# Kernel tuning notes

Measured on AMD Instinct MI355X. Metric: run time of the kernel, lower is better.

Reference implementation:

```python
import math
import jax, jax.numpy as jnp
import numpy as np

B, S, D, H, L = 2, 2048, 1024, 16, 4
HD = D // H  # head_dim = 64


def setup_inputs() -> dict:
    key = jax.random.key(0)
    ks = jax.random.split(key, 7)
    scale = 0.02
    return {
        "x": jax.random.normal(ks[0], (B, S, D), jnp.float32),
        "past_q": jax.random.normal(ks[1], (B, H, S, L, HD), jnp.float32),
        "past_v": jax.random.normal(ks[2], (B, H, S, L, HD), jnp.float32),
        "Wq": jax.random.normal(ks[3], (D, D), jnp.float32) * scale,
        "bq": jnp.zeros((D,), jnp.float32),
        "Wo": jax.random.normal(ks[4], (D, D), jnp.float32) * scale,
        "bo": jnp.zeros((D,), jnp.float32),
    }


def reference(x, past_q, past_v, Wq, bq, Wo, bo):
    b, s, d = x.shape
    # q_proj then split heads -> [B,H,S,hd]
    q = (x @ Wq.T + bq).reshape(b, s, H, HD).transpose(0, 2, 1, 3)
    v = x.reshape(b, s, H, HD).transpose(0, 2, 1, 3)
    inv = 1.0 / math.sqrt(HD)
    # token scores: Q used as both query and key, causal mask
    token_scores = jnp.einsum("bhqd,bhkd->bhqk", q, q) * inv
    causal = jnp.triu(jnp.ones((s, s), bool), k=1)
    token_scores = jnp.where(causal, -jnp.inf, token_scores)
    # memory scores: elementwise mul-sum over L cached layers -> [B,H,S,L]
    mem_scores = jnp.einsum("bhsd,bhsld->bhsl", q, past_q) * inv
    scores = jnp.concatenate([token_scores, mem_scores], axis=-1)  # [B,H,S,S+L]
    weights = jax.nn.softmax(scores, axis=-1)
    tw, mw = weights[..., :s], weights[..., s:]
    token_ctx = jnp.einsum("bhqk,bhkd->bhqd", tw, v)
    mem_ctx = jnp.einsum("bhsl,bhsld->bhsd", mw, past_v)
    ctx = (token_ctx + mem_ctx).transpose(0, 2, 1, 3).reshape(b, s, d)
    return jax.nn.gelu(ctx @ Wo.T + bo, approximate=False)
```

## Files before the change

kernel.cpp:

```cpp
#include <hip/hip_runtime.h>
#include <hip/hip_bf16.h>
#include <math.h>

#define S_LEN 2048
#define DIM   1024
#define NH    16
#define NL    4
#define NB    2
#define PARTS_PER_BH 80
#define ALPHA 0.42466086f

typedef __attribute__((ext_vector_type(8))) short bf16x8;
typedef __attribute__((ext_vector_type(4))) float f32x4;
typedef unsigned short u16;

__device__ __forceinline__ float bf2f(u16 u) {
  union { unsigned int i; float f; } x; x.i = ((unsigned int)u) << 16; return x.f;
}
__device__ __forceinline__ u16 f2bf(float f) {
  union { float f; unsigned int i; } x; x.f = f;
  unsigned int r = x.i + 0x7fffu + ((x.i >> 16) & 1u);
  return (u16)(r >> 16);
}
__device__ __forceinline__ u16 f2bfq(float f) {
  __hip_bfloat16 h = __float2bfloat16(f);
  return *reinterpret_cast<u16*>(&h);
}

__device__ __forceinline__ void g2l16(const void* g, void* l) {
  __builtin_amdgcn_global_load_lds(
      (const __attribute__((address_space(1))) void*)g,
      (__attribute__((address_space(3))) void*)l, 16, 0, 0);
}

__global__ __launch_bounds__(256)
void cvt_all(const float* __restrict__ x, const float* __restrict__ wq,
             const float* __restrict__ wo, u16* __restrict__ ox,
             u16* __restrict__ owq, u16* __restrict__ owo, int n4x, int n4w) {
  int i = blockIdx.x * blockDim.x + threadIdx.x;
  const float* src; u16* dst; int j;
  if (i < n4x)            { src = x;  dst = ox;  j = i; }
  else if (i < n4x + n4w) { src = wq; dst = owq; j = i - n4x; }
  else                    { src = wo; dst = owo; j = i - n4x - n4w;
                            if (j >= n4w) return; }
  float4 v = ((const float4*)src)[j];
  ushort4 o;
  o.x = f2bf(v.x); o.y = f2bf(v.y); o.z = f2bf(v.z); o.w = f2bf(v.w);
  ((ushort4*)dst)[j] = o;
}

template <bool GELU, typename OT>
__global__ __launch_bounds__(256)
void gemm_bt(const u16* __restrict__ A, const u16* __restrict__ Bt,
             const float* __restrict__ bias, OT* __restrict__ C,
             int M, int N, int K, float oscale) {
  __shared__ u16 As[128 * 64];
  __shared__ u16 Bs[64 * 64];
  const int lane = threadIdx.x & 63, wave = threadIdx.x >> 6;
  const int ln = lane & 15, g = lane >> 4;
  const int m0 = blockIdx.y * 128, n0 = blockIdx.x * 64;
  const int wm = wave >> 1, wn = wave & 1;
  f32x4 acc[4][2] = {};

  for (int k0 = 0; k0 < K; k0 += 64) {
    __syncthreads();
#pragma unroll
    for (int rd = 0; rd < 6; ++rd) {
      int ch = rd * 4 + wave;
      if (ch < 16) {
        int flat = ch * 1024 + lane * 16;
        int row = flat >> 7;
        int within = (flat & 127) ^ ((row & 7) << 4);
        g2l16((const char*)A + ((size_t)(m0 + row) * K + k0) * 2 + within,
              (char*)As + ch * 1024);
      } else {
        int flat = (ch - 16) * 1024 + lane * 16;
        int row = flat >> 7;
        int within = (flat & 127) ^ ((row & 7) << 4);
        g2l16((const char*)Bt + ((size_t)(n0 + row) * K + k0) * 2 + within,
              (char*)Bs + (ch - 16) * 1024);
      }
    }
    __syncthreads();
#pragma unroll
    for (int kc = 0; kc < 2; ++kc) {
      bf16x8 af[4], bfr[2];
#pragma unroll
      for (int i = 0; i < 4; ++i) {
        int ra = wm * 64 + i * 16 + ln;
        af[i] = *(const bf16x8*)((const char*)As + ra * 128 +
                                 ((kc * 64 + g * 16) ^ ((ra & 7) << 4)));
      }
#pragma unroll
      for (int j = 0; j < 2; ++j) {
        int rb = wn * 32 + j * 16 + ln;
        bfr[j] = *(const bf16x8*)((const char*)Bs + rb * 128 +
                                  ((kc * 64 + g * 16) ^ ((rb & 7) << 4)));
      }
#pragma unroll
      for (int i = 0; i < 4; ++i)
#pragma unroll
        for (int j = 0; j < 2; ++j)
          acc[i][j] = __builtin_amdgcn_mfma_f32_16x16x32_bf16(af[i], bfr[j], acc[i][j], 0, 0, 0);
    }
  }

#pragma unroll
  for (int j = 0; j < 2; ++j) {
    int gc = n0 + wn * 32 + j * 16 + ln;
    float bv = bias[gc];
#pragma unroll
    for (int i = 0; i < 4; ++i) {
      int gr0 = m0 + wm * 64 + i * 16 + g * 4;
#pragma unroll
      for (int r = 0; r < 4; ++r) {
        float v = acc[i][j][r] + bv;
        if constexpr (GELU) v = 0.5f * v * (1.0f + erff(v * 0.70710678118f));
        v *= oscale;
        if constexpr (sizeof(OT) == 2) C[(size_t)(gr0 + r) * N + gc] = (OT)f2bf(v);
        else                           C[(size_t)(gr0 + r) * N + gc] = (OT)v;
      }
    }
  }
}

__global__ __launch_bounds__(256)
void attn(const u16* __restrict__ Q, const u16* __restrict__ Xb,
          u16* __restrict__ CTXP, float* __restrict__ MP, float* __restrict__ LP) {
  __shared__ u16 Ks[2][64 * 64];
  __shared__ u16 Vt[2][64 * 64];
  __shared__ u16 Pw[4][16 * 64];

  const int lane = threadIdx.x & 63, wave = threadIdx.x >> 6;
  const int ln = lane & 15, g = lane >> 4;
  const int h = blockIdx.y, b = blockIdx.z;

  const int p = blockIdx.x;
  int qt, chunk;
  if (p < 8)       { qt = p;                          chunk = 0; }
  else if (p < 24) { int i = p - 8;  qt = 8 + (i >> 1);  chunk = i & 1; }
  else if (p < 48) { int i = p - 24; qt = 16 + i / 3;    chunk = i % 3; }
  else             { int i = p - 48; qt = 24 + (i >> 2); chunk = i & 3; }
  const int kt0 = chunk * 8;
  const int kt1e = kt0 + 8 < qt + 1 ? kt0 + 8 : qt + 1;

  const size_t qrow = (size_t)b * S_LEN + qt * 64 + wave * 16 + ln;
  const bf16x8 qa0 = *(const bf16x8*)(Q + qrow * DIM + h * 64 + g * 8);
  const bf16x8 qa1 = *(const bf16x8*)(Q + qrow * DIM + h * 64 + 32 + g * 8);

  f32x4 acc[4] = {};
  float m_run = -INFINITY;
  float l_run = 0.f;

  const int tid = threadIdx.x;
  const int vr0 = (tid >> 3) * 2;
  const int vc0 = (tid & 7) * 8;
#define VSWZ(c) ((((c) ^ ((c) >> 3)) & 7) << 4)

  {
    const u16* xsrc = Xb + ((size_t)b * S_LEN + kt0 * 64 + vr0) * DIM + h * 64 + vc0;
    bf16x8 r0 = *(const bf16x8*)xsrc;
    bf16x8 r1 = *(const bf16x8*)(xsrc + DIM);
#pragma unroll
    for (int rd = 0; rd < 2; ++rd) {
      int ch = rd * 4 + wave;
      int flat = ch * 1024 + lane * 16;
      int row = flat >> 7;
      int within = (flat & 127) ^ ((row & 7) << 4);
      g2l16((const char*)Q + (((size_t)b * S_LEN + kt0 * 64 + row) * DIM + h * 64) * 2 + within,
            (char*)Ks[0] + ch * 1024);
    }
#pragma unroll
    for (int j = 0; j < 8; ++j) {
      int c = vc0 + j;
      unsigned int pack = (unsigned int)(u16)r0[j] | ((unsigned int)(u16)r1[j] << 16);
      *(unsigned int*)((char*)Vt[0] + c * 128 + ((vr0 * 2) ^ VSWZ(c))) = pack;
    }
  }
  __syncthreads();

  for (int kt = kt0; kt < kt1e; ++kt) {
    const int cur = (kt - kt0) & 1, nxt = cur ^ 1;
    const bool more = (kt + 1 < kt1e);
    bf16x8 nr0, nr1;
    if (more) {
      const u16* xsrc = Xb + ((size_t)b * S_LEN + (kt + 1) * 64 + vr0) * DIM + h * 64 + vc0;
      nr0 = *(const bf16x8*)xsrc;
      nr1 = *(const bf16x8*)(xsrc + DIM);
#pragma unroll
      for (int rd = 0; rd < 2; ++rd) {
        int ch = rd * 4 + wave;
        int flat = ch * 1024 + lane * 16;
        int row = flat >> 7;
        int within = (flat & 127) ^ ((row & 7) << 4);
        g2l16((const char*)Q + (((size_t)b * S_LEN + (kt + 1) * 64 + row) * DIM + h * 64) * 2 + within,
              (char*)Ks[nxt] + ch * 1024);
      }
      __builtin_amdgcn_sched_barrier(0);
    }

    float pv_[4][4];
#pragma unroll
    for (int sub = 0; sub < 4; ++sub) {
      int kr = sub * 16 + ln;
      bf16x8 kb0 = *(const bf16x8*)((const char*)Ks[cur] + kr * 128 + ((g * 16) ^ ((kr & 7) << 4)));
      bf16x8 kb1 = *(const bf16x8*)((const char*)Ks[cur] + kr * 128 + ((64 + g * 16) ^ ((kr & 7) << 4)));
      f32x4 c = {};
      c = __builtin_amdgcn_mfma_f32_16x16x32_bf16(kb0, qa0, c, 0, 0, 0);
      c = __builtin_amdgcn_mfma_f32_16x16x32_bf16(kb1, qa1, c, 0, 0, 0);
      if (kt == qt) {
#pragma unroll
        for (int r = 0; r < 4; ++r) {
          int key = sub * 16 + g * 4 + r;
          int qi = wave * 16 + ln;
          pv_[sub][r] = (key > qi) ? -INFINITY : c[r];
        }
      } else {
#pragma unroll
        for (int r = 0; r < 4; ++r) pv_[sub][r] = c[r];
      }
    }

    float pmax = pv_[0][0];
#pragma unroll
    for (int sub = 0; sub < 4; ++sub)
#pragma unroll
      for (int r = 0; r < 4; ++r) pmax = fmaxf(pmax, pv_[sub][r]);
    pmax = fmaxf(pmax, __shfl_xor(pmax, 16));
    pmax = fmaxf(pmax, __shfl_xor(pmax, 32));

    if (!__all(pmax <= m_run + 8.0f)) {
      float m_new = fmaxf(m_run, pmax);
      float scl = exp2f(m_run - m_new);
      m_run = m_new;
      l_run *= scl;
#pragma unroll
      for (int r = 0; r < 4; ++r) {
        float s = __shfl(scl, g * 4 + r);
#pragma unroll
        for (int ns = 0; ns < 4; ++ns) acc[ns][r] *= s;
      }
    }

    float lsum = 0.f;
#pragma unroll
    for (int sub = 0; sub < 4; ++sub)
#pragma unroll
      for (int r = 0; r < 4; ++r) {
        pv_[sub][r] = exp2f(pv_[sub][r] - m_run);
        lsum += pv_[sub][r];
      }
    lsum += __shfl_xor(lsum, 16);
    lsum += __shfl_xor(lsum, 32);
    l_run += lsum;

#pragma unroll
    for (int sub = 0; sub < 4; ++sub) {
      uint2 val;
      val.x = (unsigned int)f2bfq(pv_[sub][0]) | ((unsigned int)f2bfq(pv_[sub][1]) << 16);
      val.y = (unsigned int)f2bfq(pv_[sub][2]) | ((unsigned int)f2bfq(pv_[sub][3]) << 16);
      *(uint2*)((char*)Pw[wave] + ln * 128 + ((sub * 32 + g * 8) ^ ((ln & 7) << 4))) = val;
    }

    bf16x8 pa0 = *(const bf16x8*)((const char*)Pw[wave] + ln * 128 + ((g * 16) ^ ((ln & 7) << 4)));
    bf16x8 pa1 = *(const bf16x8*)((const char*)Pw[wave] + ln * 128 + ((64 + g * 16) ^ ((ln & 7) << 4)));
#pragma unroll
    for (int ns = 0; ns < 4; ++ns) {
      int vr = ns * 16 + ln;
      bf16x8 vb0 = *(const bf16x8*)((const char*)Vt[cur] + vr * 128 + ((g * 16) ^ VSWZ(vr)));
      bf16x8 vb1 = *(const bf16x8*)((const char*)Vt[cur] + vr * 128 + ((64 + g * 16) ^ VSWZ(vr)));
      acc[ns] = __builtin_amdgcn_mfma_f32_16x16x32_bf16(pa0, vb0, acc[ns], 0, 0, 0);
      acc[ns] = __builtin_amdgcn_mfma_f32_16x16x32_bf16(pa1, vb1, acc[ns], 0, 0, 0);
    }

    if (more) {
#pragma unroll
      for (int j = 0; j < 8; ++j) {
        int c = vc0 + j;
        unsigned int pack = (unsigned int)(u16)nr0[j] | ((unsigned int)(u16)nr1[j] << 16);
        *(unsigned int*)((char*)Vt[nxt] + c * 128 + ((vr0 * 2) ^ VSWZ(c))) = pack;
      }
    }
    __syncthreads();
  }

  const size_t slot = ((size_t)(b * NH + h)) * PARTS_PER_BH + p;
#pragma unroll
  for (int ns = 0; ns < 4; ++ns)
#pragma unroll
    for (int r = 0; r < 4; ++r) {
      int qr = wave * 16 + g * 4 + r;
      CTXP[slot * 4096 + (size_t)qr * 64 + ns * 16 + ln] = f2bfq(acc[ns][r]);
    }
  if (lane < 16) {
    MP[slot * 64 + wave * 16 + lane] = m_run;
    LP[slot * 64 + wave * 16 + lane] = l_run;
  }
}

__global__ __launch_bounds__(256)
void finalize(const u16* __restrict__ Q, const float* __restrict__ PQ,
              const float* __restrict__ PV, const u16* __restrict__ CTXP,
              const float* __restrict__ MP, const float* __restrict__ LP,
              u16* __restrict__ Cout) {
  const int lane = threadIdx.x & 63, wave = threadIdx.x >> 6;
  const size_t row = (size_t)blockIdx.x * 4 + wave;
  const int s = (int)(row & (S_LEN - 1));
  const int h = (int)((row >> 11) & (NH - 1));
  const int b = (int)(row >> 15);

  const int qt = s >> 6, G = qt >> 3, parts = G + 1;
  const int baseG[4] = {0, 8, 24, 48};
  const int p0 = baseG[G] + (qt & 7) * parts;
  const size_t slot0 = ((size_t)(b * NH + h)) * PARTS_PER_BH + p0;
  const int sr = s & 63;

  float mc[4], lc[4];
  float m_tok = -INFINITY;
#pragma unroll
  for (int c = 0; c < 4; ++c)
    if (c < parts) {
      mc[c] = MP[(slot0 + c) * 64 + sr];
      lc[c] = LP[(slot0 + c) * 64 + sr];
      m_tok = fmaxf(m_tok, mc[c]);
    }
  float l_tok = 0.f, cd = 0.f;
#pragma unroll
  for (int c = 0; c < 4; ++c)
    if (c < parts) {
      float w = exp2f(mc[c] - m_tok);
      l_tok += w * lc[c];
      cd += w * bf2f(CTXP[(slot0 + c) * 4096 + (size_t)sr * 64 + lane]);
    }

  const float qd = bf2f(Q[((size_t)b * S_LEN + s) * DIM + h * 64 + lane]);
  const float* pq = PQ + row * (NL * 64);
  const float* pv = PV + row * (NL * 64);
  float msc[NL];
  float m_fin = m_tok;
#pragma unroll
  for (int lm = 0; lm < NL; ++lm) {
    float prod = qd * pq[lm * 64 + lane];
#pragma unroll
    for (int o = 1; o < 64; o <<= 1) prod += __shfl_xor(prod, o);
    msc[lm] = prod * ALPHA;
    m_fin = fmaxf(m_fin, msc[lm]);
  }
  const float a = exp2f(m_tok - m_fin);
  float l_fin = l_tok * a;
  cd *= a;
#pragma unroll
  for (int lm = 0; lm < NL; ++lm) {
    float w = exp2f(msc[lm] - m_fin);
    l_fin += w;
    cd += w * pv[lm * 64 + lane];
  }
  Cout[((size_t)b * S_LEN + s) * DIM + h * 64 + lane] = f2bf(cd / l_fin);
}

extern "C" void kernel_launch(void* const* d_in, const int* in_sizes, int n_in,
                              void* d_out, int out_size, void* d_ws, size_t ws_size,
                              hipStream_t stream) {
  const float* x  = (const float*)d_in[0];
  const float* pq = (const float*)d_in[1];
  const float* pv = (const float*)d_in[2];
  const float* Wq = (const float*)d_in[3];
  const float* bq = (const float*)d_in[4];
  const float* Wo = (const float*)d_in[5];
  const float* bo = (const float*)d_in[6];
  float* out = (float*)d_out;

  const int M = NB * S_LEN;
  u16*   Qws  = (u16*)d_ws;
  u16*   Cws  = Qws + (size_t)M * DIM;
  u16*   xbf  = Cws + (size_t)M * DIM;
  u16*   Wqbf = xbf + (size_t)M * DIM;
  u16*   Wobf = Wqbf + (size_t)DIM * DIM;
  u16*   CTXP = Wobf + (size_t)DIM * DIM;
  float* MP   = (float*)(CTXP + (size_t)NB * NH * PARTS_PER_BH * 4096);
  float* LP   = MP + (size_t)NB * NH * PARTS_PER_BH * 64;

  const int n4x = M * DIM / 4, n4w = DIM * DIM / 4;
  cvt_all<<<(n4x + 2 * n4w + 255) / 256, 256, 0, stream>>>(
      x, Wq, Wo, xbf, Wqbf, Wobf, n4x, n4w);

  gemm_bt<false, u16><<<dim3(DIM / 64, M / 128), 256, 0, stream>>>(
      xbf, Wqbf, bq, Qws, M, DIM, DIM, ALPHA);
  attn<<<dim3(PARTS_PER_BH, NH, NB), 256, 0, stream>>>(Qws, xbf, CTXP, MP, LP);
  finalize<<<NB * NH * S_LEN / 4, 256, 0, stream>>>(Qws, pq, pv, CTXP, MP, LP, Cws);
  gemm_bt<true, float><<<dim3(DIM / 64, M / 128), 256, 0, stream>>>(
      Cws, Wobf, bo, out, M, DIM, DIM, 1.0f);
}
```

Measured before the change: 137.8 us.

## Double-buffer GEMM LDS tiles and defer softmax cross-lane reductions in attention

The GEMM kernel now keeps two LDS buffers, loading the next K tile while MFMAs consume the current one, which removes one barrier per iteration and overlaps global loads with compute. In the attention kernel the per-row max is only combined across lanes when a rescale is triggered, and the row-sum is kept per lane and reduced once after the loop. This removes shuffles from the hot loop. Double buffering doubles GEMM LDS use, which may lower occupancy.

```diff
diff --git a/kernel.cpp b/kernel.cpp
--- a/kernel.cpp
+++ b/kernel.cpp
@@ -54,16 +54,15 @@
 void gemm_bt(const u16* __restrict__ A, const u16* __restrict__ Bt,
              const float* __restrict__ bias, OT* __restrict__ C,
              int M, int N, int K, float oscale) {
-  __shared__ u16 As[128 * 64];
-  __shared__ u16 Bs[64 * 64];
+  __shared__ u16 As[2][128 * 64];
+  __shared__ u16 Bs[2][64 * 64];
   const int lane = threadIdx.x & 63, wave = threadIdx.x >> 6;
   const int ln = lane & 15, g = lane >> 4;
   const int m0 = blockIdx.y * 128, n0 = blockIdx.x * 64;
   const int wm = wave >> 1, wn = wave & 1;
   f32x4 acc[4][2] = {};
 
-  for (int k0 = 0; k0 < K; k0 += 64) {
-    __syncthreads();
+  auto stage = [&](int buf, int k0) {
 #pragma unroll
     for (int rd = 0; rd < 6; ++rd) {
       int ch = rd * 4 + wave;
@@ -72,29 +71,36 @@
         int row = flat >> 7;
         int within = (flat & 127) ^ ((row & 7) << 4);
         g2l16((const char*)A + ((size_t)(m0 + row) * K + k0) * 2 + within,
-              (char*)As + ch * 1024);
+              (char*)As[buf] + ch * 1024);
       } else {
         int flat = (ch - 16) * 1024 + lane * 16;
         int row = flat >> 7;
         int within = (flat & 127) ^ ((row & 7) << 4);
         g2l16((const char*)Bt + ((size_t)(n0 + row) * K + k0) * 2 + within,
-              (char*)Bs + (ch - 16) * 1024);
-      }
-    }
-    __syncthreads();
+              (char*)Bs[buf] + (ch - 16) * 1024);
+      }
+    }
+  };
+
+  stage(0, 0);
+  __syncthreads();
+  const int NT = K / 64;
+  for (int t = 0; t < NT; ++t) {
+    const int cur = t & 1;
+    if (t + 1 < NT) stage(cur ^ 1, (t + 1) * 64);
 #pragma unroll
     for (int kc = 0; kc < 2; ++kc) {
       bf16x8 af[4], bfr[2];
 #pragma unroll
       for (int i = 0; i < 4; ++i) {
         int ra = wm * 64 + i * 16 + ln;
-        af[i] = *(const bf16x8*)((const char*)As + ra * 128 +
+        af[i] = *(const bf16x8*)((const char*)As[cur] + ra * 128 +
                                  ((kc * 64 + g * 16) ^ ((ra & 7) << 4)));
       }
 #pragma unroll
       for (int j = 0; j < 2; ++j) {
         int rb = wn * 32 + j * 16 + ln;
-        bfr[j] = *(const bf16x8*)((const char*)Bs + rb * 128 +
+        bfr[j] = *(const bf16x8*)((const char*)Bs[cur] + rb * 128 +
                                   ((kc * 64 + g * 16) ^ ((rb & 7) << 4)));
       }
 #pragma unroll
@@ -103,6 +109,7 @@
         for (int j = 0; j < 2; ++j)
           acc[i][j] = __builtin_amdgcn_mfma_f32_16x16x32_bf16(af[i], bfr[j], acc[i][j], 0, 0, 0);
     }
+    __syncthreads();
   }
 
 #pragma unroll
@@ -150,7 +157,7 @@
 
   f32x4 acc[4] = {};
   float m_run = -INFINITY;
-  float l_run = 0.f;
+  float l_part = 0.f;
 
   const int tid = threadIdx.x;
   const int vr0 = (tid >> 3) * 2;
@@ -221,19 +228,21 @@
       }
     }
 
-    float pmax = pv_[0][0];
-#pragma unroll
-    for (int sub = 0; sub < 4; ++sub)
-#pragma unroll
-      for (int r = 0; r < 4; ++r) pmax = fmaxf(pmax, pv_[sub][r]);
-    pmax = fmaxf(pmax, __shfl_xor(pmax, 16));
-    pmax = fmaxf(pmax, __shfl_xor(pmax, 32));
+    float t0 = fmaxf(fmaxf(pv_[0][0], pv_[0][1]), pv_[0][2]);
+    float t1 = fmaxf(fmaxf(pv_[0][3], pv_[1][0]), pv_[1][1]);
+    float t2 = fmaxf(fmaxf(pv_[1][2], pv_[1][3]), pv_[2][0]);
+    float t3 = fmaxf(fmaxf(pv_[2][1], pv_[2][2]), pv_[2][3]);
+    float t4 = fmaxf(fmaxf(pv_[3][0], pv_[3][1]), pv_[3][2]);
+    float pmax = fmaxf(fmaxf(fmaxf(t0, t1), fmaxf(t2, t3)),
+                       fmaxf(t4, pv_[3][3]));
 
     if (!__all(pmax <= m_run + 8.0f)) {
-      float m_new = fmaxf(m_run, pmax);
+      float fm = fmaxf(pmax, __shfl_xor(pmax, 16));
+      fm = fmaxf(fm, __shfl_xor(fm, 32));
+      float m_new = fmaxf(m_run, fm);
       float scl = exp2f(m_run - m_new);
       m_run = m_new;
-      l_run *= scl;
+      l_part *= scl;
 #pragma unroll
       for (int r = 0; r < 4; ++r) {
         float s = __shfl(scl, g * 4 + r);
@@ -242,17 +251,15 @@
       }
     }
 
-    float lsum = 0.f;
+    float ls = 0.f;
 #pragma unroll
     for (int sub = 0; sub < 4; ++sub)
 #pragma unroll
       for (int r = 0; r < 4; ++r) {
         pv_[sub][r] = exp2f(pv_[sub][r] - m_run);
-        lsum += pv_[sub][r];
-      }
-    lsum += __shfl_xor(lsum, 16);
-    lsum += __shfl_xor(lsum, 32);
-    l_run += lsum;
+        ls += pv_[sub][r];
+      }
+    l_part += ls;
 
 #pragma unroll
     for (int sub = 0; sub < 4; ++sub) {
@@ -283,6 +290,10 @@
     }
     __syncthreads();
   }
+
+  float l_run = l_part;
+  l_run += __shfl_xor(l_run, 16);
+  l_run += __shfl_xor(l_run, 32);
 
   const size_t slot = ((size_t)(b * NH + h)) * PARTS_PER_BH + p;
 #pragma unroll
```

New measurement: 142.7 us. +3.6%, slower.

## Double-buffer GEMM LDS tiles and load attention K directly from global memory

Applied to the files above, without the earlier changes.

The GEMM now double-buffers its A/B shared-memory tiles, issuing the next K-tile's async loads before computing on the current one, so there is one barrier per iteration instead of two. In the attention kernel the K tile is no longer staged through LDS; each lane reads its K fragments straight from global memory (Q), which removes the LDS traffic and shared-memory footprint. The trade-off is that global-load latency now sits directly in front of the QK^T MFMAs with no prefetch, and the GEMM uses twice the LDS, which may reduce occupancy.

```diff
diff --git a/kernel.cpp b/kernel.cpp
--- a/kernel.cpp
+++ b/kernel.cpp
@@ -54,16 +54,15 @@
 void gemm_bt(const u16* __restrict__ A, const u16* __restrict__ Bt,
              const float* __restrict__ bias, OT* __restrict__ C,
              int M, int N, int K, float oscale) {
-  __shared__ u16 As[128 * 64];
-  __shared__ u16 Bs[64 * 64];
+  __shared__ u16 As[2][128 * 64];
+  __shared__ u16 Bs[2][64 * 64];
   const int lane = threadIdx.x & 63, wave = threadIdx.x >> 6;
   const int ln = lane & 15, g = lane >> 4;
   const int m0 = blockIdx.y * 128, n0 = blockIdx.x * 64;
   const int wm = wave >> 1, wn = wave & 1;
   f32x4 acc[4][2] = {};
 
-  for (int k0 = 0; k0 < K; k0 += 64) {
-    __syncthreads();
+  auto stage = [&](int buf, int k0) {
 #pragma unroll
     for (int rd = 0; rd < 6; ++rd) {
       int ch = rd * 4 + wave;
@@ -72,29 +71,36 @@
         int row = flat >> 7;
         int within = (flat & 127) ^ ((row & 7) << 4);
         g2l16((const char*)A + ((size_t)(m0 + row) * K + k0) * 2 + within,
-              (char*)As + ch * 1024);
+              (char*)As[buf] + ch * 1024);
       } else {
         int flat = (ch - 16) * 1024 + lane * 16;
         int row = flat >> 7;
         int within = (flat & 127) ^ ((row & 7) << 4);
         g2l16((const char*)Bt + ((size_t)(n0 + row) * K + k0) * 2 + within,
-              (char*)Bs + (ch - 16) * 1024);
-      }
-    }
-    __syncthreads();
+              (char*)Bs[buf] + (ch - 16) * 1024);
+      }
+    }
+  };
+
+  stage(0, 0);
+  __syncthreads();
+  const int NT = K / 64;
+  for (int t = 0; t < NT; ++t) {
+    const int cur = t & 1;
+    if (t + 1 < NT) stage(cur ^ 1, (t + 1) * 64);
 #pragma unroll
     for (int kc = 0; kc < 2; ++kc) {
       bf16x8 af[4], bfr[2];
 #pragma unroll
       for (int i = 0; i < 4; ++i) {
         int ra = wm * 64 + i * 16 + ln;
-        af[i] = *(const bf16x8*)((const char*)As + ra * 128 +
+        af[i] = *(const bf16x8*)((const char*)As[cur] + ra * 128 +
                                  ((kc * 64 + g * 16) ^ ((ra & 7) << 4)));
       }
 #pragma unroll
       for (int j = 0; j < 2; ++j) {
         int rb = wn * 32 + j * 16 + ln;
-        bfr[j] = *(const bf16x8*)((const char*)Bs + rb * 128 +
+        bfr[j] = *(const bf16x8*)((const char*)Bs[cur] + rb * 128 +
                                   ((kc * 64 + g * 16) ^ ((rb & 7) << 4)));
       }
 #pragma unroll
@@ -103,6 +109,7 @@
         for (int j = 0; j < 2; ++j)
           acc[i][j] = __builtin_amdgcn_mfma_f32_16x16x32_bf16(af[i], bfr[j], acc[i][j], 0, 0, 0);
     }
+    __syncthreads();
   }
 
 #pragma unroll
@@ -127,7 +134,6 @@
 __global__ __launch_bounds__(256)
 void attn(const u16* __restrict__ Q, const u16* __restrict__ Xb,
           u16* __restrict__ CTXP, float* __restrict__ MP, float* __restrict__ LP) {
-  __shared__ u16 Ks[2][64 * 64];
   __shared__ u16 Vt[2][64 * 64];
   __shared__ u16 Pw[4][16 * 64];
 
@@ -148,6 +154,8 @@
   const bf16x8 qa0 = *(const bf16x8*)(Q + qrow * DIM + h * 64 + g * 8);
   const bf16x8 qa1 = *(const bf16x8*)(Q + qrow * DIM + h * 64 + 32 + g * 8);
 
+  const u16* Kbase = Q + ((size_t)b * S_LEN) * DIM + h * 64 + g * 8;
+
   f32x4 acc[4] = {};
   float m_run = -INFINITY;
   float l_run = 0.f;
@@ -161,15 +169,6 @@
     const u16* xsrc = Xb + ((size_t)b * S_LEN + kt0 * 64 + vr0) * DIM + h * 64 + vc0;
     bf16x8 r0 = *(const bf16x8*)xsrc;
     bf16x8 r1 = *(const bf16x8*)(xsrc + DIM);
-#pragma unroll
-    for (int rd = 0; rd < 2; ++rd) {
-      int ch = rd * 4 + wave;
-      int flat = ch * 1024 + lane * 16;
-      int row = flat >> 7;
-      int within = (flat & 127) ^ ((row & 7) << 4);
-      g2l16((const char*)Q + (((size_t)b * S_LEN + kt0 * 64 + row) * DIM + h * 64) * 2 + within,
-            (char*)Ks[0] + ch * 1024);
-    }
 #pragma unroll
     for (int j = 0; j < 8; ++j) {
       int c = vc0 + j;
@@ -187,24 +186,14 @@
       const u16* xsrc = Xb + ((size_t)b * S_LEN + (kt + 1) * 64 + vr0) * DIM + h * 64 + vc0;
       nr0 = *(const bf16x8*)xsrc;
       nr1 = *(const bf16x8*)(xsrc + DIM);
-#pragma unroll
-      for (int rd = 0; rd < 2; ++rd) {
-        int ch = rd * 4 + wave;
-        int flat = ch * 1024 + lane * 16;
-        int row = flat >> 7;
-        int within = (flat & 127) ^ ((row & 7) << 4);
-        g2l16((const char*)Q + (((size_t)b * S_LEN + (kt + 1) * 64 + row) * DIM + h * 64) * 2 + within,
-              (char*)Ks[nxt] + ch * 1024);
-      }
-      __builtin_amdgcn_sched_barrier(0);
     }
 
     float pv_[4][4];
 #pragma unroll
     for (int sub = 0; sub < 4; ++sub) {
-      int kr = sub * 16 + ln;
-      bf16x8 kb0 = *(const bf16x8*)((const char*)Ks[cur] + kr * 128 + ((g * 16) ^ ((kr & 7) << 4)));
-      bf16x8 kb1 = *(const bf16x8*)((const char*)Ks[cur] + kr * 128 + ((64 + g * 16) ^ ((kr & 7) << 4)));
+      const u16* kp = Kbase + (size_t)(kt * 64 + sub * 16 + ln) * DIM;
+      bf16x8 kb0 = *(const bf16x8*)kp;
+      bf16x8 kb1 = *(const bf16x8*)(kp + 32);
       f32x4 c = {};
       c = __builtin_amdgcn_mfma_f32_16x16x32_bf16(kb0, qa0, c, 0, 0, 0);
       c = __builtin_amdgcn_mfma_f32_16x16x32_bf16(kb1, qa1, c, 0, 0, 0);
```

Result: slower. 176.4 us (+28.0%).
